# Performance work log

Measured on AMD Instinct MI355X. Metric: run time of the kernel, lower is better.

## Reference

```python
import jax, jax.numpy as jnp
import numpy as np
from jax import lax

B, C, H, W = 16, 256, 64, 64
HID = 128
EQ = 256


def _lstm_dir(x, Wih, Whh, b, hidden):
    # x: [N, T, D]; PyTorch gate order i, f, g, o
    N = x.shape[0]
    h0 = jnp.zeros((N, hidden), x.dtype)
    c0 = jnp.zeros((N, hidden), x.dtype)
    xT = jnp.swapaxes(x, 0, 1)  # [T, N, D]
    pre = jnp.einsum('tnd,gd->tng', xT, Wih) + b  # precompute input projection

    def step(carry, xt):
        h, c = carry
        g = xt + h @ Whh.T
        i, f, gg, o = jnp.split(g, 4, axis=-1)
        c = jax.nn.sigmoid(f) * c + jax.nn.sigmoid(i) * jnp.tanh(gg)
        h = jax.nn.sigmoid(o) * jnp.tanh(c)
        return (h, c), h

    _, hs = lax.scan(step, (h0, c0), pre)
    return jnp.swapaxes(hs, 0, 1)  # [N, T, hidden]


def _bilstm(x, Wih_f, Whh_f, b_f, Wih_b, Whh_b, b_b, hidden):
    hf = _lstm_dir(x, Wih_f, Whh_f, b_f, hidden)
    hb = _lstm_dir(x[:, ::-1], Wih_b, Whh_b, b_b, hidden)[:, ::-1]
    return jnp.concatenate([hf, hb], axis=-1)


def setup_inputs() -> dict:
    key = jax.random.key(0)
    ks = jax.random.split(key, 16)
    s = 1.0 / np.sqrt(HID)
    d = {}
    d['input'] = jax.random.normal(ks[0], (B, C, H, W), jnp.float32)
    # horizontal LSTM (input_size=C)
    d['h_Wih_f'] = jax.random.uniform(ks[1], (4 * HID, C), jnp.float32, -s, s)
    d['h_Whh_f'] = jax.random.uniform(ks[2], (4 * HID, HID), jnp.float32, -s, s)
    d['h_b_f'] = jax.random.uniform(ks[3], (4 * HID,), jnp.float32, -s, s)
    d['h_Wih_b'] = jax.random.uniform(ks[4], (4 * HID, C), jnp.float32, -s, s)
    d['h_Whh_b'] = jax.random.uniform(ks[5], (4 * HID, HID), jnp.float32, -s, s)
    d['h_b_b'] = jax.random.uniform(ks[6], (4 * HID,), jnp.float32, -s, s)
    # vertical LSTM (input_size=2*HID)
    d['v_Wih_f'] = jax.random.uniform(ks[7], (4 * HID, 2 * HID), jnp.float32, -s, s)
    d['v_Whh_f'] = jax.random.uniform(ks[8], (4 * HID, HID), jnp.float32, -s, s)
    d['v_b_f'] = jax.random.uniform(ks[9], (4 * HID,), jnp.float32, -s, s)
    d['v_Wih_b'] = jax.random.uniform(ks[10], (4 * HID, 2 * HID), jnp.float32, -s, s)
    d['v_Whh_b'] = jax.random.uniform(ks[11], (4 * HID, HID), jnp.float32, -s, s)
    d['v_b_b'] = jax.random.uniform(ks[12], (4 * HID,), jnp.float32, -s, s)
    # 1x1 convs (no bias)
    d['Wr'] = jax.random.normal(ks[13], (EQ, 2 * HID), jnp.float32) * 0.05
    d['Wl'] = jax.random.normal(ks[14], (EQ, C), jnp.float32) * 0.05
    d['alpha'] = jnp.zeros((1,), jnp.float32) + 0.5  # nonzero so output depends on attention
    return d


def reference(input, h_Wih_f, h_Whh_f, h_b_f, h_Wih_b, h_Whh_b, h_b_b,
              v_Wih_f, v_Whh_f, v_b_f, v_Wih_b, v_Whh_b, v_b_b, Wr, Wl, alpha):
    b, c, h, w = input.shape
    # transpose(1,3): [B, W, H, C]; horizontal LSTM runs over H for each w
    x = jnp.transpose(input, (0, 3, 2, 1))  # [B, W, H, C]
    xh = x.reshape(b * w, h, c)
    hor = _bilstm(xh, h_Wih_f, h_Whh_f, h_b_f, h_Wih_b, h_Whh_b, h_b_b, HID)
    hor = hor.reshape(b, w, h, 2 * HID)  # == torch horizontal_feature
    # vertical LSTM: sequences over W for each h-index
    xv = jnp.transpose(hor, (0, 2, 1, 3)).reshape(b * h, w, 2 * HID)
    ver = _bilstm(xv, v_Wih_f, v_Whh_f, v_b_f, v_Wih_b, v_Whh_b, v_b_b, HID)
    ver = ver.reshape(b, h, w, 2 * HID)  # vf[b, hi, wi, :]
    # torch: stack dim=2 -> [B, W, H, 2Hd]; permute(0,3,1,2) -> [B, 2Hd, W, H]
    vf = jnp.transpose(ver, (0, 3, 2, 1))  # [B, 2Hd, W, H]
    vf = jnp.einsum('oc,bcwh->bowh', Wr, vf)  # conv_right 1x1
    vf = vf.reshape(b, EQ, h * w)
    vf = jax.nn.softmax(vf, axis=2)
    # left branch
    q = jnp.einsum('oc,bchw->bohw', Wl, input)
    q_avg = jnp.mean(q, axis=(2, 3)).reshape(b, 1, EQ)
    q_avg = jax.nn.softmax(q_avg, axis=2)
    attention = jnp.matmul(q_avg, vf).reshape(b, 1, h, w)
    attention = jax.nn.sigmoid(attention)
    out = input * attention
    return out * alpha + input
```

## Files before the change

kernel.cpp:

```cpp
#include <hip/hip_runtime.h>
#include <hip/hip_bf16.h>

typedef unsigned short u16;
typedef unsigned int u32;
typedef unsigned char u8;
typedef long long ll8;
typedef __attribute__((ext_vector_type(8))) short s8v;
typedef __attribute__((ext_vector_type(4))) float f4v;

__device__ __forceinline__ float b2f(u16 u) {
  union { u32 i; float f; } v; v.i = ((u32)u) << 16; return v.f;
}
__device__ __forceinline__ u16 f2b(float f) {
  union { float f; u32 i; } v; v.f = f;
  u32 r = v.i + 0x7FFFu + ((v.i >> 16) & 1u);
  return (u16)(r >> 16);
}
__device__ __forceinline__ float rcpf(float x) { return __builtin_amdgcn_rcpf(x); }
__device__ __forceinline__ float ex2(float x) {
#if __has_builtin(__builtin_amdgcn_exp2f)
  return __builtin_amdgcn_exp2f(x);
#else
  return exp2f(x);
#endif
}
__device__ __forceinline__ float sigf(float x) { return rcpf(1.0f + __expf(-x)); }
template<bool HI>
__device__ __forceinline__ u32 pkfp8(float a, float b, u32 old) {
  return (u32)__builtin_amdgcn_cvt_pk_fp8_f32(a, b, (int)old, HI);
}
__device__ __forceinline__ u8 f2f8(float x) { return (u8)(pkfp8<false>(x, x, 0) & 0xffu); }
template<int S>
__device__ __forceinline__ float f8tof(u32 v) {
#if __has_builtin(__builtin_amdgcn_cvt_f32_fp8)
  return __builtin_amdgcn_cvt_f32_fp8((int)v, S);
#else
  u8 b = (u8)(v >> (8 * S));
  u32 s = (b >> 7) & 1u, e = (b >> 3) & 15u, m = b & 7u;
  union { u32 i; float f; } r;
  if (e) r.i = (s << 31) | ((e + 120u) << 23) | (m << 20);
  else { r.f = (float)m * 0.001953125f; r.i |= s << 31; }
  return r.f;
#endif
}

#define GS_IFO 1.4426950408889634f
#define GS_G   2.8853900817779268f

__device__ __forceinline__ void gl_lds16(const void* g, void* l) {
  __builtin_amdgcn_global_load_lds(
      (const __attribute__((address_space(1))) u32*)g,
      (__attribute__((address_space(3))) u32*)l, 16, 0, 0);
}

struct CvtArgs {
  const float* src[9];
  u8* dst[9];
  int n4[9];
  int scl[9];
  int sh[9];
};
__global__ __launch_bounds__(256) void k_cvt(CvtArgs a) {
  int seg = blockIdx.y;
  int i = blockIdx.x * 256 + threadIdx.x;
  if (i >= a.n4[seg]) return;
  float4 v = ((const float4*)a.src[seg])[i];
  float s;
  if (a.scl[seg] == 2) {
    s = GS_IFO;
  } else {
    int r = i >> a.sh[seg];
    s = (((r >> 7) & 3) == 2) ? GS_G : GS_IFO;
  }
  v.x *= s; v.y *= s; v.z *= s; v.w *= s;
  u32 p = pkfp8<false>(v.x, v.y, 0);
  p = pkfp8<true>(v.z, v.w, p);
  ((u32*)a.dst[seg])[i] = p;
}

__global__ __launch_bounds__(256) void k_tin(const float* __restrict__ in,
                                             u8* __restrict__ A8,
                                             float* __restrict__ meansum) {
  int b = blockIdx.z, h = blockIdx.y, c0 = blockIdx.x * 64;
  int t = threadIdx.x, lane = t & 63, q = t >> 6;
  __shared__ u8 lT[64][68];
  const float* src = in + ((b * 256 + c0) * 64 + h) * 64;
#pragma unroll 4
  for (int i = 0; i < 16; ++i) {
    int cl = q * 16 + i;
    float v = src[cl * 4096 + lane];
    lT[cl][lane] = f2f8(v);
    float s = v;
#pragma unroll
    for (int off = 32; off; off >>= 1) s += __shfl_xor(s, off);
    if (lane == 0) atomicAdd(&meansum[b * 256 + c0 + cl], s);
  }
  __syncthreads();
  u8* dst = A8 + (b * 4096 + h) * 256 + c0;
#pragma unroll 4
  for (int i = 0; i < 16; ++i) {
    int w = q * 16 + i;
    dst[w * 16384 + lane] = lT[lane][w];
  }
}

__global__ __launch_bounds__(256) void k_qavg(const float* __restrict__ meansum,
                                              const float* __restrict__ Wl,
                                              float* __restrict__ qavg) {
  int b = blockIdx.x, t = threadIdx.x;
  __shared__ float mean[256];
  __shared__ float red[256];
  mean[t] = meansum[b * 256 + t] * (1.0f / 4096.0f);
  __syncthreads();
  const float* wr = Wl + t * 256;
  float acc = 0.0f;
  for (int c = 0; c < 256; ++c) acc = fmaf(wr[c], mean[c], acc);
  red[t] = acc; __syncthreads();
  for (int s = 128; s; s >>= 1) { if (t < s) red[t] = fmaxf(red[t], red[t + s]); __syncthreads(); }
  float mx = red[0]; __syncthreads();
  float e = __expf(acc - mx);
  red[t] = e; __syncthreads();
  for (int s = 128; s; s >>= 1) { if (t < s) red[t] += red[t + s]; __syncthreads(); }
  qavg[b * 256 + t] = e / red[0];
}

__global__ __launch_bounds__(256, 2) void k_gemm8(const u8* __restrict__ A,
                                                  const u8* __restrict__ W,
                                                  u8* __restrict__ out,
                                                  float* __restrict__ Zsum) {
  int nwg = gridDim.x;
  int q = nwg >> 3;
  int bid = blockIdx.x;
  int swz = (bid & 7) * q + (bid >> 3);
  int mt = swz >> 1, nt = swz & 1;
  int mb = mt << 7, nb = nt << 7;
  int t = threadIdx.x, lane = t & 63, wid = t >> 6;
  int laneg = lane & 15, lk = lane >> 4;
  __shared__ __align__(16) u8 lA[128][256];
  __shared__ __align__(16) u8 lW[128][256];
  {
    int rl = lane >> 4;
    int unit = lane & 15;
#pragma unroll
    for (int i = 0; i < 8; ++i) {
      int rb4 = ((wid << 3) + i) << 2;
      int r = rb4 + rl;
      int usA = unit ^ (r & 7);
      gl_lds16(A + (mb + r) * 256 + (usA << 4), &lA[rb4][0]);
      gl_lds16(W + (nb + r) * 256 + (usA << 4), &lW[rb4][0]);
    }
  }
  __syncthreads();
  f4v acc[4][4] = {};
  int wm = wid >> 1, wn = wid & 1;
#pragma unroll
  for (int kk = 0; kk < 8; ++kk) {
    ll8 af[4], bf[4];
#pragma unroll
    for (int m = 0; m < 4; ++m) {
      int r = (wm << 6) + (m << 4) + laneg;
      int us = ((kk << 1) + (lk >> 1)) ^ (r & 7);
      af[m] = *(const ll8*)&lA[r][(us << 4) + ((lk & 1) << 3)];
    }
#pragma unroll
    for (int n = 0; n < 4; ++n) {
      int r = (wn << 6) + (n << 4) + laneg;
      int us = ((kk << 1) + (lk >> 1)) ^ (r & 7);
      bf[n] = *(const ll8*)&lW[r][(us << 4) + ((lk & 1) << 3)];
    }
#pragma unroll
    for (int m = 0; m < 4; ++m)
#pragma unroll
      for (int n = 0; n < 4; ++n)
        acc[m][n] = __builtin_amdgcn_mfma_f32_16x16x32_fp8_fp8(af[m], bf[n], acc[m][n], 0, 0, 0);
  }
#pragma unroll
  for (int n = 0; n < 4; ++n) {
    int col = nb + (wn << 6) + (n << 4) + laneg;
    float csum = 0.f;
#pragma unroll
    for (int m = 0; m < 4; ++m) {
      int row0 = mb + (wm << 6) + (m << 4) + (lk << 2);
#pragma unroll
      for (int j = 0; j < 4; ++j) {
        float e = ex2(acc[m][n][j]);
        csum += e;
        out[(row0 + j) * 256 + col] = f2f8(e);
      }
    }
    csum += __shfl_xor(csum, 16);
    csum += __shfl_xor(csum, 32);
    if (lk == 0) atomicAdd(&Zsum[((mb >> 12) << 8) + col], csum);
  }
}

__global__ __launch_bounds__(512, 1) void k_recur_f(const u8* __restrict__ X8,
                                                    const u8* __restrict__ Wi8,
                                                    const u8* __restrict__ Wh8d,
                                                    const float* __restrict__ bias_f,
                                                    const float* __restrict__ bias_b,
                                                    u8* __restrict__ outb) {
  int dir = blockIdx.y;
  int s0 = blockIdx.x << 4;
  int t = threadIdx.x, lane = t & 63, w = t >> 6;
  int laneg = lane & 15, lk = lane >> 4;
  const u8* Wd = Wh8d + dir * 65536;
  const u8* Wi = Wi8 + dir * 131072;
  const float* bia = dir ? bias_b : bias_f;
  int hc = w << 4;
  ll8 bfr[4][4];
#pragma unroll
  for (int g = 0; g < 4; ++g)
#pragma unroll
    for (int kk = 0; kk < 4; ++kk)
      bfr[g][kk] = *(const ll8*)(Wd + (g * 128 + hc + laneg) * 128 + kk * 32 + lk * 8);
  ll8 ifr[4][8];
#pragma unroll
  for (int g = 0; g < 4; ++g)
#pragma unroll
    for (int kk = 0; kk < 8; ++kk)
      ifr[g][kk] = *(const ll8*)(Wi + (g * 128 + hc + laneg) * 256 + kk * 32 + lk * 8);
  float bval[4];
#pragma unroll
  for (int g = 0; g < 4; ++g)
    bval[g] = bia[g * 128 + hc + laneg] * ((g == 2) ? GS_G : GS_IFO);

  __shared__ __align__(16) u8 hb[2][16][144];
  __shared__ __align__(16) u8 xb[3][16][256];
  for (int i = t; i < 2 * 16 * 144; i += 512) ((u8*)hb)[i] = 0;

  float cs[4] = {0.f, 0.f, 0.f, 0.f};
  int tc0 = dir ? 63 : 0;
  int dstep = dir ? -1 : 1;
  int srw = (w << 2) + (lane >> 4);
  int c16 = lane & 15;
  const u8* xsrc = X8 + (s0 + srw) * 16384 + ((c16 ^ (srw & 7)) << 4);
  int srow = t >> 5;
  int schunk = t & 31;
  int rowb = ((s0 >> 6) << 12) + (s0 & 63);
  if (w < 4) {
    gl_lds16(xsrc + tc0 * 256, &xb[0][w << 2][0]);
    gl_lds16(xsrc + ((tc0 + dstep) & 63) * 256, &xb[1][w << 2][0]);
  }
  __syncthreads();
  int cur = 0;
  for (int st = 0; st < 64; ++st) {
    int tc = tc0 + st * dstep;
    if (st) {
      int pr = tc - dstep;
      u32 hv = *(const u32*)&hb[cur][srow][schunk << 2];
      *(u32*)(outb + (rowb + pr * 64 + srow) * 256 + (dir << 7) + (schunk << 2)) = hv;
    }
    if (w < 4 && st < 62) {
      int tn = tc0 + (st + 2) * dstep;
      gl_lds16(xsrc + tn * 256, &xb[(st + 2) % 3][w << 2][0]);
    }
    f4v acc[4];
#pragma unroll
    for (int g = 0; g < 4; ++g)
      acc[g] = (f4v){bval[g], bval[g], bval[g], bval[g]};
    {
      const u8* xrow = &xb[st % 3][laneg][0];
      ll8 xf[8];
#pragma unroll
      for (int kk = 0; kk < 8; ++kk)
        xf[kk] = *(const ll8*)&xrow[((((kk << 1) + (lk >> 1)) ^ (laneg & 7)) << 4) + ((lk & 1) << 3)];
#pragma unroll
      for (int g = 0; g < 4; ++g)
#pragma unroll
        for (int kk = 0; kk < 8; ++kk)
          acc[g] = __builtin_amdgcn_mfma_f32_16x16x32_fp8_fp8(xf[kk], ifr[g][kk], acc[g], 0, 0, 0);
    }
    {
      ll8 afr[4];
#pragma unroll
      for (int kk = 0; kk < 4; ++kk)
        afr[kk] = *(const ll8*)&hb[cur][laneg][kk * 32 + lk * 8];
#pragma unroll
      for (int g = 0; g < 4; ++g)
#pragma unroll
        for (int kk = 0; kk < 4; ++kk)
          acc[g] = __builtin_amdgcn_mfma_f32_16x16x32_fp8_fp8(afr[kk], bfr[g][kk], acc[g], 0, 0, 0);
    }
    int nxt = cur ^ 1;
#pragma unroll
    for (int j = 0; j < 4; ++j) {
      float iv = rcpf(1.0f + ex2(-acc[0][j]));
      float fv = rcpf(1.0f + ex2(-acc[1][j]));
      float gv = 1.0f - 2.0f * rcpf(1.0f + ex2(acc[2][j]));
      float ov = rcpf(1.0f + ex2(-acc[3][j]));
      float c = fv * cs[j] + iv * gv;
      cs[j] = c;
      float th = 1.0f - 2.0f * rcpf(1.0f + ex2(c * GS_G));
      hb[nxt][(lk << 2) + j][hc + laneg] = f2f8(ov * th);
    }
    asm volatile("s_waitcnt lgkmcnt(0)" ::: "memory");
    __builtin_amdgcn_s_barrier();
    cur = nxt;
  }
  {
    int pr = tc0 + 63 * dstep;
    u32 hv = *(const u32*)&hb[cur][srow][schunk << 2];
    *(u32*)(outb + (rowb + pr * 64 + srow) * 256 + (dir << 7) + (schunk << 2)) = hv;
  }
}

__global__ __launch_bounds__(256) void k_attfin(const u8* __restrict__ VF8,
                                                const float* __restrict__ qavg,
                                                const float* __restrict__ Z,
                                                const float* __restrict__ in,
                                                const float* __restrict__ alpha,
                                                float* __restrict__ out) {
  int bx = blockIdx.x;
  int b = bx >> 6;
  int sp0 = (bx & 63) << 6;
  int t = threadIdx.x, lane = t & 63, wid = t >> 6;
  __shared__ __align__(16) float lwo[256];
  __shared__ float fac[64];
  lwo[t] = qavg[b * 256 + t] / Z[b * 256 + t];
  __syncthreads();
  float4 wo = *(const float4*)&lwo[lane * 4];
  int rowbase = b * 4096 + sp0;
#pragma unroll 4
  for (int i = 0; i < 16; ++i) {
    int r = wid * 16 + i;
    u32 v = *(const u32*)&VF8[(rowbase + r) * 256 + lane * 4];
    float p = wo.x * f8tof<0>(v) + wo.y * f8tof<1>(v) +
              wo.z * f8tof<2>(v) + wo.w * f8tof<3>(v);
#pragma unroll
    for (int off = 32; off; off >>= 1) p += __shfl_xor(p, off);
    if (lane == 0) fac[r] = p;
  }
  __syncthreads();
  float al = alpha[0];
  if (t < 64) fac[t] = 1.0f + al * sigf(fac[t]);
  __syncthreads();
  int sp = t & 63;
  float f = fac[sp];
  const float* ip = in + (long)b * 1048576 + sp0 + sp;
  float* op = out + (long)b * 1048576 + sp0 + sp;
  int c0 = t >> 6;
#pragma unroll 8
  for (int c = c0; c < 256; c += 4) {
    op[c * 4096] = ip[c * 4096] * f;
  }
}

extern "C" void kernel_launch(void* const* d_in, const int* in_sizes, int n_in,
                              void* d_out, int out_size, void* d_ws, size_t ws_size,
                              hipStream_t stream) {
  const float* input   = (const float*)d_in[0];
  const float* h_Wih_f = (const float*)d_in[1];
  const float* h_Whh_f = (const float*)d_in[2];
  const float* h_b_f   = (const float*)d_in[3];
  const float* h_Wih_b = (const float*)d_in[4];
  const float* h_Whh_b = (const float*)d_in[5];
  const float* h_b_b   = (const float*)d_in[6];
  const float* v_Wih_f = (const float*)d_in[7];
  const float* v_Whh_f = (const float*)d_in[8];
  const float* v_b_f   = (const float*)d_in[9];
  const float* v_Wih_b = (const float*)d_in[10];
  const float* v_Whh_b = (const float*)d_in[11];
  const float* v_b_b   = (const float*)d_in[12];
  const float* Wr      = (const float*)d_in[13];
  const float* Wl      = (const float*)d_in[14];
  const float* alphap  = (const float*)d_in[15];

  char* ws = (char*)d_ws;
  u8*  Ah8   = (u8*)(ws + 0);
  u8*  VF8   = (u8*)(ws + 33554432);
  u8*  Wh8   = (u8*)(ws + 67108864);
  u8*  Wv8   = (u8*)(ws + 67371008);
  u8*  WhhH8 = (u8*)(ws + 67633152);
  u8*  WhhV8 = (u8*)(ws + 67764224);
  u8*  Wrb8  = (u8*)(ws + 67895296);
  float* meansum = (float*)(ws + 67960832);
  float* qavg    = (float*)(ws + 67977216);
  float* pZ      = (float*)(ws + 67993600);
  u8*  Av8 = (u8*)d_out;
  u8*  Ar8 = Ah8;

  (void)hipMemsetAsync(meansum, 0, 3 * 16384, stream);

  CvtArgs ca;
  ca.src[0] = h_Wih_f; ca.dst[0] = Wh8;           ca.n4[0] = 32768; ca.scl[0] = 1; ca.sh[0] = 6;
  ca.src[1] = h_Wih_b; ca.dst[1] = Wh8 + 131072;  ca.n4[1] = 32768; ca.scl[1] = 1; ca.sh[1] = 6;
  ca.src[2] = v_Wih_f; ca.dst[2] = Wv8;           ca.n4[2] = 32768; ca.scl[2] = 1; ca.sh[2] = 6;
  ca.src[3] = v_Wih_b; ca.dst[3] = Wv8 + 131072;  ca.n4[3] = 32768; ca.scl[3] = 1; ca.sh[3] = 6;
  ca.src[4] = h_Whh_f; ca.dst[4] = WhhH8;         ca.n4[4] = 16384; ca.scl[4] = 1; ca.sh[4] = 5;
  ca.src[5] = h_Whh_b; ca.dst[5] = WhhH8 + 65536; ca.n4[5] = 16384; ca.scl[5] = 1; ca.sh[5] = 5;
  ca.src[6] = v_Whh_f; ca.dst[6] = WhhV8;         ca.n4[6] = 16384; ca.scl[6] = 1; ca.sh[6] = 5;
  ca.src[7] = v_Whh_b; ca.dst[7] = WhhV8 + 65536; ca.n4[7] = 16384; ca.scl[7] = 1; ca.sh[7] = 5;
  ca.src[8] = Wr;      ca.dst[8] = Wrb8;          ca.n4[8] = 16384; ca.scl[8] = 2; ca.sh[8] = 6;
  k_cvt<<<dim3(128, 9), 256, 0, stream>>>(ca);

  k_tin<<<dim3(4, 64, 16), 256, 0, stream>>>(input, Ah8, meansum);
  k_qavg<<<16, 256, 0, stream>>>(meansum, Wl, qavg);

  k_recur_f<<<dim3(64, 2), 512, 0, stream>>>(Ah8, Wh8, WhhH8, h_b_f, h_b_b, Av8);
  k_recur_f<<<dim3(64, 2), 512, 0, stream>>>(Av8, Wv8, WhhV8, v_b_f, v_b_b, Ar8);
  k_gemm8<<<1024, 256, 0, stream>>>(Ar8, Wrb8, VF8, pZ);

  k_attfin<<<1024, 256, 0, stream>>>(VF8, qavg, pZ, input, alphap, (float*)d_out);
}
```

Before: 315.6 us.

## Software-pipeline input projection one step ahead and fuse gate reciprocals

The fp8 LSTM recurrence kernel now computes the input-projection MFMAs for step t+1 during step t, so only the recurrent h@Whh MFMAs sit on the critical path before the gate math. The x staging ring grows from three to four LDS buffers, with prefetch three steps ahead and an explicit vmcnt wait. Gate math is reworked algebraically to merge sigmoid and tanh reciprocals, leaving fewer rcp instructions per element. Unused bf16 helpers are removed. The costs are more LDS, extra live accumulator registers, and slightly different rounding.

Result: faster. 307.2 us (-2.7%).

```diff
diff --git a/kernel.cpp b/kernel.cpp
--- a/kernel.cpp
+++ b/kernel.cpp
@@ -5,17 +5,8 @@
 typedef unsigned int u32;
 typedef unsigned char u8;
 typedef long long ll8;
-typedef __attribute__((ext_vector_type(8))) short s8v;
 typedef __attribute__((ext_vector_type(4))) float f4v;
 
-__device__ __forceinline__ float b2f(u16 u) {
-  union { u32 i; float f; } v; v.i = ((u32)u) << 16; return v.f;
-}
-__device__ __forceinline__ u16 f2b(float f) {
-  union { float f; u32 i; } v; v.f = f;
-  u32 r = v.i + 0x7FFFu + ((v.i >> 16) & 1u);
-  return (u16)(r >> 16);
-}
 __device__ __forceinline__ float rcpf(float x) { return __builtin_amdgcn_rcpf(x); }
 __device__ __forceinline__ float ex2(float x) {
 #if __has_builtin(__builtin_amdgcn_exp2f)
@@ -226,7 +217,7 @@
     bval[g] = bia[g * 128 + hc + laneg] * ((g == 2) ? GS_G : GS_IFO);
 
   __shared__ __align__(16) u8 hb[2][16][144];
-  __shared__ __align__(16) u8 xb[3][16][256];
+  __shared__ __align__(16) u8 xb[4][16][256];
   for (int i = t; i < 2 * 16 * 144; i += 512) ((u8*)hb)[i] = 0;
 
   float cs[4] = {0.f, 0.f, 0.f, 0.f};
@@ -240,27 +231,57 @@
   int rowb = ((s0 >> 6) << 12) + (s0 & 63);
   if (w < 4) {
     gl_lds16(xsrc + tc0 * 256, &xb[0][w << 2][0]);
-    gl_lds16(xsrc + ((tc0 + dstep) & 63) * 256, &xb[1][w << 2][0]);
-  }
-  __syncthreads();
+    gl_lds16(xsrc + (tc0 + dstep) * 256, &xb[1][w << 2][0]);
+    gl_lds16(xsrc + (tc0 + 2 * dstep) * 256, &xb[2][w << 2][0]);
+  }
+  __syncthreads();
+  f4v nacc[4];
+#pragma unroll
+  for (int g = 0; g < 4; ++g)
+    nacc[g] = (f4v){bval[g], bval[g], bval[g], bval[g]};
+  {
+    const u8* xrow = &xb[0][laneg][0];
+    ll8 xf[8];
+#pragma unroll
+    for (int kk = 0; kk < 8; ++kk)
+      xf[kk] = *(const ll8*)&xrow[((((kk << 1) + (lk >> 1)) ^ (laneg & 7)) << 4) + ((lk & 1) << 3)];
+#pragma unroll
+    for (int g = 0; g < 4; ++g)
+#pragma unroll
+      for (int kk = 0; kk < 8; ++kk)
+        nacc[g] = __builtin_amdgcn_mfma_f32_16x16x32_fp8_fp8(xf[kk], ifr[g][kk], nacc[g], 0, 0, 0);
+  }
   int cur = 0;
   for (int st = 0; st < 64; ++st) {
     int tc = tc0 + st * dstep;
+    f4v acc[4];
+#pragma unroll
+    for (int g = 0; g < 4; ++g) acc[g] = nacc[g];
     if (st) {
       int pr = tc - dstep;
       u32 hv = *(const u32*)&hb[cur][srow][schunk << 2];
       *(u32*)(outb + (rowb + pr * 64 + srow) * 256 + (dir << 7) + (schunk << 2)) = hv;
     }
-    if (w < 4 && st < 62) {
-      int tn = tc0 + (st + 2) * dstep;
-      gl_lds16(xsrc + tn * 256, &xb[(st + 2) % 3][w << 2][0]);
-    }
-    f4v acc[4];
-#pragma unroll
-    for (int g = 0; g < 4; ++g)
-      acc[g] = (f4v){bval[g], bval[g], bval[g], bval[g]};
+    if (w < 4 && st < 61) {
+      gl_lds16(xsrc + (tc0 + (st + 3) * dstep) * 256, &xb[(st + 3) & 3][w << 2][0]);
+    }
     {
-      const u8* xrow = &xb[st % 3][laneg][0];
+      ll8 afr[4];
+#pragma unroll
+      for (int kk = 0; kk < 4; ++kk)
+        afr[kk] = *(const ll8*)&hb[cur][laneg][kk * 32 + lk * 8];
+#pragma unroll
+      for (int g = 0; g < 4; ++g)
+#pragma unroll
+        for (int kk = 0; kk < 4; ++kk)
+          acc[g] = __builtin_amdgcn_mfma_f32_16x16x32_fp8_fp8(afr[kk], bfr[g][kk], acc[g], 0, 0, 0);
+    }
+    if (st < 63) {
+      asm volatile("s_waitcnt vmcnt(4)" ::: "memory");
+#pragma unroll
+      for (int g = 0; g < 4; ++g)
+        nacc[g] = (f4v){bval[g], bval[g], bval[g], bval[g]};
+      const u8* xrow = &xb[(st + 1) & 3][laneg][0];
       ll8 xf[8];
 #pragma unroll
       for (int kk = 0; kk < 8; ++kk)
@@ -269,30 +290,21 @@
       for (int g = 0; g < 4; ++g)
 #pragma unroll
         for (int kk = 0; kk < 8; ++kk)
-          acc[g] = __builtin_amdgcn_mfma_f32_16x16x32_fp8_fp8(xf[kk], ifr[g][kk], acc[g], 0, 0, 0);
-    }
-    {
-      ll8 afr[4];
-#pragma unroll
-      for (int kk = 0; kk < 4; ++kk)
-        afr[kk] = *(const ll8*)&hb[cur][laneg][kk * 32 + lk * 8];
-#pragma unroll
-      for (int g = 0; g < 4; ++g)
-#pragma unroll
-        for (int kk = 0; kk < 4; ++kk)
-          acc[g] = __builtin_amdgcn_mfma_f32_16x16x32_fp8_fp8(afr[kk], bfr[g][kk], acc[g], 0, 0, 0);
+          nacc[g] = __builtin_amdgcn_mfma_f32_16x16x32_fp8_fp8(xf[kk], ifr[g][kk], nacc[g], 0, 0, 0);
     }
     int nxt = cur ^ 1;
 #pragma unroll
     for (int j = 0; j < 4; ++j) {
-      float iv = rcpf(1.0f + ex2(-acc[0][j]));
-      float fv = rcpf(1.0f + ex2(-acc[1][j]));
-      float gv = 1.0f - 2.0f * rcpf(1.0f + ex2(acc[2][j]));
-      float ov = rcpf(1.0f + ex2(-acc[3][j]));
-      float c = fv * cs[j] + iv * gv;
+      float Y = ex2(-acc[0][j]);
+      float V = ex2(-acc[1][j]);
+      float X = ex2(acc[2][j]);
+      float W = ex2(-acc[3][j]);
+      float ig = (X - 1.0f) * rcpf((1.0f + Y) * (X + 1.0f));
+      float c = cs[j] * rcpf(1.0f + V) + ig;
       cs[j] = c;
-      float th = 1.0f - 2.0f * rcpf(1.0f + ex2(c * GS_G));
-      hb[nxt][(lk << 2) + j][hc + laneg] = f2f8(ov * th);
+      float Z = ex2(c * GS_G);
+      float h = (Z - 1.0f) * rcpf((1.0f + W) * (Z + 1.0f));
+      hb[nxt][(lk << 2) + j][hc + laneg] = f2f8(h);
     }
     asm volatile("s_waitcnt lgkmcnt(0)" ::: "memory");
     __builtin_amdgcn_s_barrier();
```
